# Optimization experiments

Measured on AMD Instinct MI355X. Metric: run time of the kernel, lower is better.

Reference implementation:

```python
import jax, jax.numpy as jnp
import numpy as np

# Module hyperparameters (from init_kwargs)
H, F = 8, 32            # num_heads, attention_filters
RY, RX = 3, 3           # spatial_radius
PH, PW = 2 * RY + 1, 2 * RX + 1
S = PH * PW             # patch_size = 49
HF = H * F


def setup_inputs() -> dict:
    key = jax.random.key(0)
    ks = jax.random.split(key, 6)
    B, Y, X, C = 4, 64, 64, 256
    x = jax.random.normal(ks[0], (B, Y, X, C), jnp.float32)
    # 1x1 conv kernels == dense matrices over the channel dim (no bias)
    Wq = jax.random.normal(ks[1], (C, HF), jnp.float32) / np.sqrt(C)
    Wk = jax.random.normal(ks[2], (C, HF), jnp.float32) / np.sqrt(C)
    Wv = jax.random.normal(ks[3], (C, HF), jnp.float32) / np.sqrt(C)
    Wo = jax.random.normal(ks[4], (HF, C), jnp.float32) / np.sqrt(HF)
    pos_emb = jax.random.normal(ks[5], (S, HF), jnp.float32) * 0.02
    return {"x": x, "Wq": Wq, "Wk": Wk, "Wv": Wv, "Wo": Wo, "pos_emb": pos_emb}


def reference(x, Wq, Wk, Wv, Wo, pos_emb):
    B, Y, X, C = x.shape
    dtype = x.dtype
    # 1x1 conv projections
    Q = x @ Wq                       # (B,Y,X,HF)
    K = x @ Wk
    V = x @ Wv
    # clipped patch centers (borders reuse interior patches)
    cy = jnp.clip(jnp.arange(Y), RY, Y - RY - 1)   # (Y,)
    cx = jnp.clip(jnp.arange(X), RX, X - RX - 1)   # (X,)
    # query relative-position indices within its patch
    qy = jnp.arange(Y) - cy + RY
    qx = jnp.arange(X) - cx + RX
    qidx = qy[:, None] * PW + qx[None, :]          # (Y,X) in [0,S)
    Q = Q + pos_emb[qidx]                          # add query pos embedding (HF)
    Q = Q.reshape(B, Y, X, H, F)
    K = K.reshape(B, Y, X, H, F)
    V = V.reshape(B, Y, X, H, F)
    cy_g, cx_g = jnp.meshgrid(cy, cx, indexing="ij")  # (Y,X)
    scale = jnp.asarray(1.0 / np.sqrt(F), dtype)
    NEG = jnp.asarray(-1e9, dtype)
    m = jnp.full((B, Y, X, H, 1), NEG, dtype)      # running max
    l = jnp.zeros((B, Y, X, H, 1), dtype)          # running sum-exp
    acc = jnp.zeros((B, Y, X, H, F), dtype)        # running value accumulator
    dy_vec = np.arange(-RY, RY + 1)                # within-chunk offsets ('col' mode)
    for dx in range(-RX, RX + 1):                  # chunk loop over columns (7 chunks)
        ny = jnp.clip(cy_g[None, :, :] + dy_vec[:, None, None], 0, Y - 1)  # (PH,Y,X)
        nx = jnp.clip(cx_g[None, :, :] + dx, 0, X - 1)                     # (1,Y,X)
        nx = jnp.broadcast_to(nx, ny.shape)
        sidx = (dy_vec + RY) * PW + (dx + RX)      # (PH,) relative-pos indices
        # gather neighbor K/V: (B,PH,Y,X,H,F)
        Kc = K[:, ny, nx] + pos_emb[sidx].reshape(PH, 1, 1, H, F)
        Vc = V[:, ny, nx]
        sc = jnp.einsum("byxhf,bsyxhf->byxhs", Q, Kc) * scale  # (B,Y,X,H,PH)
        new_m = jnp.maximum(m, sc.max(axis=-1, keepdims=True))
        alpha = jnp.exp(m - new_m)
        p = jnp.exp(sc - new_m)
        l = l * alpha + p.sum(axis=-1, keepdims=True)
        acc = acc * alpha + jnp.einsum("byxhs,bsyxhf->byxhf", p, Vc)
        m = new_m
    out = (acc / (l + 1e-8)).reshape(B, Y, X, HF) @ Wo
    return out
```

## Files before the change

kernel.cpp:

```cpp
#include <hip/hip_runtime.h>
#include <hip/hip_bf16.h>

static constexpr int NPOS = 4 * 64 * 64;
static constexpr int CD   = 256;
static constexpr int VSTR = 16416;
#define QSCALE (0.17677669529663687f * 1.4426950408889634f)

typedef __attribute__((ext_vector_type(8))) short bf16x8;
typedef __attribute__((ext_vector_type(4))) float f32x4;

__device__ __forceinline__ float bf2f(unsigned short u) {
    return __uint_as_float((unsigned int)u << 16);
}
__device__ __forceinline__ unsigned short bfbits(float f) {
    union { __hip_bfloat16 h; unsigned short u; } cv;
    cv.h = __float2bfloat16(f);
    return cv.u;
}
__device__ __forceinline__ unsigned int packbf2(float lo, float hi) {
    union { __hip_bfloat162 h; unsigned int u; } cv;
    cv.h.x = __float2bfloat16(lo);
    cv.h.y = __float2bfloat16(hi);
    return cv.u;
}
__device__ __forceinline__ uint4 pack8(float4 a, float4 b) {
    uint4 u;
    u.x = packbf2(a.x, a.y); u.y = packbf2(a.z, a.w);
    u.z = packbf2(b.x, b.y); u.w = packbf2(b.z, b.w);
    return u;
}
__device__ __forceinline__ void pl32swap(unsigned &a, unsigned &b) {
    auto r = __builtin_amdgcn_permlane32_swap(a, b, false, false);
    a = r[0]; b = r[1];
}
__device__ __forceinline__ void pl16swap(unsigned &a, unsigned &b) {
    auto r = __builtin_amdgcn_permlane16_swap(a, b, false, false);
    a = r[0]; b = r[1];
}

__global__ __launch_bounds__(256) void convert_kernel(
    const float* __restrict__ Wq, const float* __restrict__ Wk,
    const float* __restrict__ Wv, const float* __restrict__ Wo,
    const float* __restrict__ pe,
    __hip_bfloat16* __restrict__ Wfrag,
    __hip_bfloat16* __restrict__ pebf,
    __hip_bfloat16* __restrict__ Wofrag)
{
    int t = blockIdx.x * 256 + threadIdx.x;
    if (t < 24576) {
        int L = t & 63, ng = (t >> 6) & 7, s = (t >> 9) & 7, T = t >> 12;
        int mat = T >> 1;
        const float* src = (mat == 0) ? Wq : (mat == 1) ? Wk : Wv;
        int ncol  = (T & 1) * 128 + ng * 16 + (L & 15);
        int kbase = s * 32 + (L >> 4) * 8;
        __hip_bfloat16* dst = Wfrag + ((size_t)((T * 8 + s) * 8 + ng) * 64 + L) * 8;
#pragma unroll
        for (int j = 0; j < 8; ++j)
            dst[j] = __float2bfloat16(src[(kbase + j) * 256 + ncol]);
    } else if (t < 26624) {
        int u = t - 24576;
        int L = u & 63, Tn = (u >> 6) & 3, h = u >> 8;
        int s = Tn * 16 + (L & 15);
        int kbase = (L >> 4) * 8;
        __hip_bfloat16* dst = pebf + ((size_t)((h * 4 + Tn) * 64 + L)) * 8;
#pragma unroll
        for (int j = 0; j < 8; ++j) {
            float v = (s < 49) ? pe[s * 256 + h * 32 + kbase + j] * QSCALE : 0.f;
            dst[j] = __float2bfloat16(v);
        }
    } else if (t < 34816) {
        int u = t - 26624;
        int L = u & 63, ng = (u >> 6) & 7, s = (u >> 9) & 7, T = (u >> 12) & 1;
        int ncol  = T * 128 + ng * 16 + (L & 15);
        int kbase = s * 32 + (L >> 4) * 8;
        __hip_bfloat16* dst = Wofrag + ((size_t)((T * 8 + s) * 8 + ng) * 64 + L) * 8;
#pragma unroll
        for (int j = 0; j < 8; ++j)
            dst[j] = __float2bfloat16(Wo[(kbase + j) * 256 + ncol]);
    }
}

__global__ __launch_bounds__(768, 3) void qkv_mfma(
    const float* __restrict__ x,
    const __hip_bfloat16* __restrict__ Wfrag,
    const float* __restrict__ pe,
    unsigned short* __restrict__ QA,
    unsigned short* __restrict__ Kd,
    unsigned short* __restrict__ Vt)
{
    __shared__ __align__(16) unsigned short smem[256 * 68];
    unsigned short* As = smem;
    const int t = threadIdx.x;
    const int rowbase = blockIdx.x * 64;
    const int L = t & 63;
    const int w = t >> 6;
    const int quad = L >> 4, lrow = L & 15;
    const int T = w >> 1;
    const int ngb = (w & 1) * 4;
    const int g = T >> 1;
    const int lw = w & 3;

#pragma unroll
    for (int idx = t; idx < 2048; idx += 768) {
        const int row = idx >> 5, ch8 = idx & 31;
        const float* src = x + (size_t)(rowbase + row) * CD + ch8 * 8;
        float4 f0 = ((const float4*)src)[0];
        float4 f1 = ((const float4*)src)[1];
        *(uint4*)&As[row * 264 + ch8 * 8] = pack8(f0, f1);
    }

    f32x4 acc[4][4];
#pragma unroll
    for (int i = 0; i < 4; ++i)
#pragma unroll
        for (int j = 0; j < 4; ++j) acc[i][j] = (f32x4){0.f, 0.f, 0.f, 0.f};

    const __hip_bfloat16* wbase = Wfrag + ((size_t)(T * 64 + ngb) * 64 + L) * 8;
    bf16x8 bfr[4];
#pragma unroll
    for (int j = 0; j < 4; ++j)
        bfr[j] = *(const bf16x8*)(wbase + (size_t)j * 64 * 8);

    __syncthreads();

#pragma unroll
    for (int s = 0; s < 8; ++s) {
        bf16x8 nbfr[4];
        if (s < 7) {
#pragma unroll
            for (int j = 0; j < 4; ++j)
                nbfr[j] = *(const bf16x8*)(wbase + (size_t)((s + 1) * 8 + j) * 64 * 8);
        }
#pragma unroll
        for (int i = 0; i < 4; ++i) {
            bf16x8 af = *(const bf16x8*)&As[(i * 16 + lrow) * 264 + s * 32 + quad * 8];
#pragma unroll
            for (int j = 0; j < 4; ++j)
                acc[i][j] = __builtin_amdgcn_mfma_f32_16x16x32_bf16(af, bfr[j], acc[i][j], 0, 0, 0);
        }
#pragma unroll
        for (int j = 0; j < 4; ++j) bfr[j] = nbfr[j];
    }

    __syncthreads();

    if (g == 0) {
#pragma unroll
        for (int i = 0; i < 4; ++i)
#pragma unroll
            for (int r = 0; r < 4; ++r) {
                int row = rowbase + i * 16 + quad * 4 + r;
                int yy = (row >> 6) & 63, xx = row & 63;
                int cy = min(max(yy, 3), 60), cx = min(max(xx, 3), 60);
                int qidx = (yy - cy + 3) * 7 + (xx - cx + 3);
#pragma unroll
                for (int j = 0; j < 4; ++j) {
                    int c = lw * 64 + j * 16 + lrow;
                    QA[(size_t)row * CD + c] = bfbits(acc[i][j][r] + pe[qidx * 256 + c]);
                }
            }
    } else if (g == 1) {
#pragma unroll
        for (int i = 0; i < 4; ++i)
#pragma unroll
            for (int r = 0; r < 4; ++r) {
                int row = rowbase + i * 16 + quad * 4 + r;
#pragma unroll
                for (int j = 0; j < 4; ++j) {
                    int c = lw * 64 + j * 16 + lrow;
                    Kd[(size_t)row * CD + c] = bfbits(acc[i][j][r] * QSCALE);
                }
            }
    } else {
        unsigned short* vt = smem;
#pragma unroll
        for (int i = 0; i < 4; ++i)
#pragma unroll
            for (int j = 0; j < 4; ++j) {
                int c = lw * 64 + j * 16 + lrow;
                int row0 = i * 16 + quad * 4;
                *(unsigned int*)&vt[c * 68 + row0] =
                    (unsigned int)bfbits(acc[i][j][0]) | ((unsigned int)bfbits(acc[i][j][1]) << 16);
                *(unsigned int*)&vt[c * 68 + row0 + 2] =
                    (unsigned int)bfbits(acc[i][j][2]) | ((unsigned int)bfbits(acc[i][j][3]) << 16);
            }
    }
    __syncthreads();

    if (g == 2) {
        const int t4 = t - 512;
        const int grp = t4 >> 4, lig = t4 & 15;
        const int row_off = lig * 4;
        unsigned short* vt = smem;
#pragma unroll
        for (int pass = 0; pass < 16; ++pass) {
            int c = pass * 16 + grp;
            *(ushort4*)(Vt + (size_t)c * VSTR + rowbase + row_off) =
                *(const ushort4*)&vt[c * 68 + row_off];
        }
    }
}

__global__ __launch_bounds__(512) void attn_oproj(
    const unsigned short* __restrict__ QA,
    const unsigned short* __restrict__ Kd,
    const unsigned short* __restrict__ Vt,
    const __hip_bfloat16* __restrict__ pebf,
    const __hip_bfloat16* __restrict__ Wofrag,
    float* __restrict__ out)
{
    __shared__ __align__(16) unsigned short qpes[8][16 * 72];
    __shared__ __align__(16) unsigned short At[16 * 264];
    const int t = threadIdx.x, w = t >> 6, L = t & 63;
    const int lrow = L & 15, quad = L >> 4;
    const int bid = blockIdx.x;
    const int tile = ((bid & 7) << 7) | (bid >> 3);
    const int pos0 = tile * 16;
    const int x0 = pos0 & 63;
    const int yy = (pos0 >> 6) & 63, bb = pos0 >> 12;
    const int cy = min(max(yy, 3), 60);
    const int h = w;

    const int kc0 = min(max(x0 - 8 + lrow, 0), 63);
    const int kc1 = min(max(x0 + 8 + lrow, 0), 63);
    const f32x4 zero = {0.f, 0.f, 0.f, 0.f};
    unsigned short* qp = qpes[w];

    const int cx = min(max(x0 + lrow, 3), 60) - x0 + 5;
    int qiA[4], qiB[4];
    float mkA[4], mkB[4];
#pragma unroll
    for (int r = 0; r < 4; ++r) {
        const int sl = quad * 4 + r;
        int dxa = sl - cx;
        qiA[r] = lrow * 72 + min(max(dxa, 0), 6);
        mkA[r] = ((unsigned)dxa <= 6u) ? 1.f : 0.f;
        int dxb = 16 + sl - cx;
        qiB[r] = lrow * 72 + min(max(dxb, 0), 6);
        mkB[r] = ((unsigned)dxb <= 6u) ? 1.f : 0.f;
    }

    const bf16x8 qa = *(const bf16x8*)(QA + (size_t)(pos0 + lrow) * 256 + h * 32 + quad * 8);

#pragma unroll
    for (int Tn = 0; Tn < 4; ++Tn) {
        bf16x8 bp = *(const bf16x8*)(pebf + ((size_t)((h * 4 + Tn) * 64 + L)) * 8);
        f32x4 c = __builtin_amdgcn_mfma_f32_16x16x32_bf16(bp, qa, zero, 0, 0, 0);
        *(unsigned int*)&qp[lrow * 72 + Tn * 16 + quad * 4]     = packbf2(c[0], c[1]);
        *(unsigned int*)&qp[lrow * 72 + Tn * 16 + quad * 4 + 2] = packbf2(c[2], c[3]);
    }
    __builtin_amdgcn_s_waitcnt(0xc07f);

    float lacc = 0.f;
    f32x4 oT0 = zero, oT1 = zero;
    int rowpos = bb * 4096 + (cy - 3) * 64;

    const size_t koff = h * 32 + quad * 8;
    const size_t voff0 = (size_t)(h * 32 + lrow) * VSTR + x0 - 8 + quad * 8;
    const size_t voff1 = (size_t)(h * 32 + 16 + lrow) * VSTR + x0 - 8 + quad * 8;
    bf16x8 bk0 = *(const bf16x8*)(Kd + (size_t)(rowpos + kc0) * 256 + koff);
    bf16x8 bk1 = *(const bf16x8*)(Kd + (size_t)(rowpos + kc1) * 256 + koff);
    bf16x8 bv0 = *(const bf16x8*)(Vt + voff0 + rowpos);
    bf16x8 bv1 = *(const bf16x8*)(Vt + voff1 + rowpos);

    int qpofs = 0;
    for (int dy = 0; dy < 7; ++dy) {
        const int rnext = rowpos + 64;
        bf16x8 nk0, nk1, nv0, nv1;
        if (dy < 6) {
            nk0 = *(const bf16x8*)(Kd + (size_t)(rnext + kc0) * 256 + koff);
            nk1 = *(const bf16x8*)(Kd + (size_t)(rnext + kc1) * 256 + koff);
            nv0 = *(const bf16x8*)(Vt + voff0 + rnext);
            nv1 = *(const bf16x8*)(Vt + voff1 + rnext);
        }
        f32x4 s0 = __builtin_amdgcn_mfma_f32_16x16x32_bf16(bk0, qa, zero, 0, 0, 0);
        f32x4 s1 = __builtin_amdgcn_mfma_f32_16x16x32_bf16(bk1, qa, zero, 0, 0, 0);
        float e00 = exp2f(s0[0] + bf2f(qp[qiA[0] + qpofs])) * mkA[0];
        float e01 = exp2f(s0[1] + bf2f(qp[qiA[1] + qpofs])) * mkA[1];
        float e02 = exp2f(s0[2] + bf2f(qp[qiA[2] + qpofs])) * mkA[2];
        float e03 = exp2f(s0[3] + bf2f(qp[qiA[3] + qpofs])) * mkA[3];
        float e10 = exp2f(s1[0] + bf2f(qp[qiB[0] + qpofs])) * mkB[0];
        float e11 = exp2f(s1[1] + bf2f(qp[qiB[1] + qpofs])) * mkB[1];
        float e12 = exp2f(s1[2] + bf2f(qp[qiB[2] + qpofs])) * mkB[2];
        float e13 = exp2f(s1[3] + bf2f(qp[qiB[3] + qpofs])) * mkB[3];
        lacc += ((e00 + e01) + (e02 + e03)) + ((e10 + e11) + (e12 + e13));

        unsigned p0 = packbf2(e00, e01), p1 = packbf2(e02, e03);
        unsigned z0 = packbf2(e10, e11), z1 = packbf2(e12, e13);
        pl32swap(p0, z0);
        pl16swap(p0, z0);
        pl32swap(p1, z1);
        pl16swap(p1, z1);
        union { unsigned u[4]; bf16x8 v; } pb;
        pb.u[0] = p0; pb.u[1] = p1; pb.u[2] = z0; pb.u[3] = z1;

        oT0 = __builtin_amdgcn_mfma_f32_16x16x32_bf16(bv0, pb.v, oT0, 0, 0, 0);
        oT1 = __builtin_amdgcn_mfma_f32_16x16x32_bf16(bv1, pb.v, oT1, 0, 0, 0);
        bk0 = nk0; bk1 = nk1; bv0 = nv0; bv1 = nv1;
        rowpos = rnext;
        qpofs += 7;
    }

    lacc += __shfl_xor(lacc, 16);
    lacc += __shfl_xor(lacc, 32);
    const float inv = 1.f / (lacc + 1e-8f);

    {
        const int base = lrow * 264 + h * 32 + quad * 4;
        *(unsigned int*)&At[base]          = packbf2(oT0[0] * inv, oT0[1] * inv);
        *(unsigned int*)&At[base + 2]      = packbf2(oT0[2] * inv, oT0[3] * inv);
        *(unsigned int*)&At[base + 16]     = packbf2(oT1[0] * inv, oT1[1] * inv);
        *(unsigned int*)&At[base + 16 + 2] = packbf2(oT1[2] * inv, oT1[3] * inv);
    }
    __syncthreads();

    const int T = w >> 2;
    const int ngb = (w & 3) * 2;
    f32x4 acc[2];
    acc[0] = zero; acc[1] = zero;

#pragma unroll
    for (int s = 0; s < 8; ++s) {
        bf16x8 bfr[2];
#pragma unroll
        for (int j = 0; j < 2; ++j)
            bfr[j] = *(const bf16x8*)(Wofrag +
                      ((size_t)((T * 8 + s) * 8 + ngb + j) * 64 + L) * 8);
        bf16x8 af = *(const bf16x8*)(At + lrow * 264 + s * 32 + quad * 8);
#pragma unroll
        for (int j = 0; j < 2; ++j)
            acc[j] = __builtin_amdgcn_mfma_f32_16x16x32_bf16(af, bfr[j], acc[j], 0, 0, 0);
    }

#pragma unroll
    for (int r = 0; r < 4; ++r) {
        int row = pos0 + quad * 4 + r;
#pragma unroll
        for (int j = 0; j < 2; ++j) {
            int c = w * 32 + j * 16 + lrow;
            out[(size_t)row * CD + c] = acc[j][r];
        }
    }
}

extern "C" void kernel_launch(void* const* d_in, const int* in_sizes, int n_in,
                              void* d_out, int out_size, void* d_ws, size_t ws_size,
                              hipStream_t stream)
{
    const float* x  = (const float*)d_in[0];
    const float* Wq = (const float*)d_in[1];
    const float* Wk = (const float*)d_in[2];
    const float* Wv = (const float*)d_in[3];
    const float* Wo = (const float*)d_in[4];
    const float* pe = (const float*)d_in[5];
    float* out = (float*)d_out;

    char* ws = (char*)d_ws;
    unsigned short* QA = (unsigned short*)ws;
    unsigned short* Kd = (unsigned short*)(ws + (8u << 20));
    unsigned short* Vt = (unsigned short*)(ws + (16u << 20));
    char* fr = ws + (25u << 20) + 4096;
    __hip_bfloat16* Wfrag  = (__hip_bfloat16*)fr;
    __hip_bfloat16* pebf   = (__hip_bfloat16*)(fr + (384u << 10));
    __hip_bfloat16* Wofrag = (__hip_bfloat16*)(fr + (416u << 10));

    convert_kernel<<<136, 256, 0, stream>>>(Wq, Wk, Wv, Wo, pe, Wfrag, pebf, Wofrag);
    qkv_mfma<<<256, 768, 0, stream>>>(x, Wfrag, pe, QA, Kd, Vt);
    attn_oproj<<<1024, 512, 0, stream>>>(QA, Kd, Vt, pebf, Wofrag, out);
}
```

Baseline: 121.9 us.

## Process two adjacent query rows per attention block to share K/V loads

Each attn_oproj block now handles two vertically adjacent 16-position rows. The K/V rows they share are loaded once and fed to both tiles over 7 or 8 iterations, instead of 7 per tile. Each Wo fragment loaded in the output projection is also reused for both tiles, and the grid is halved to 512 blocks with a launch-bounds occupancy hint added. This cuts global K/V and Wo traffic, at the cost of more registers and shared memory per block and fewer blocks to fill the GPU.

New measurement: 114.6 us. 1.06x faster.

```diff
diff --git a/kernel.cpp b/kernel.cpp
--- a/kernel.cpp
+++ b/kernel.cpp
@@ -201,7 +201,7 @@
     }
 }
 
-__global__ __launch_bounds__(512) void attn_oproj(
+__global__ __launch_bounds__(512, 4) void attn_oproj(
     const unsigned short* __restrict__ QA,
     const unsigned short* __restrict__ Kd,
     const unsigned short* __restrict__ Vt,
@@ -209,22 +209,29 @@
     const __hip_bfloat16* __restrict__ Wofrag,
     float* __restrict__ out)
 {
-    __shared__ __align__(16) unsigned short qpes[8][16 * 72];
-    __shared__ __align__(16) unsigned short At[16 * 264];
+    __shared__ __align__(16) unsigned short qpes[8 * 2 * 1152];
+    __shared__ __align__(16) unsigned short At[2 * 16 * 264];
     const int t = threadIdx.x, w = t >> 6, L = t & 63;
     const int lrow = L & 15, quad = L >> 4;
     const int bid = blockIdx.x;
-    const int tile = ((bid & 7) << 7) | (bid >> 3);
-    const int pos0 = tile * 16;
-    const int x0 = pos0 & 63;
-    const int yy = (pos0 >> 6) & 63, bb = pos0 >> 12;
-    const int cy = min(max(yy, 3), 60);
+    const int p = ((bid & 7) << 6) | (bid >> 3);
+    const int b = p >> 7, ypair = (p >> 2) & 31, x0 = (p & 3) * 16;
+    const int yyA = ypair * 2;
+    const int pos0a = b * 4096 + yyA * 64 + x0;
+    const int pos0b = pos0a + 64;
+    const int cyA = min(max(yyA, 3), 60);
+    const int cyB = min(max(yyA + 1, 3), 60);
+    const int d = cyB - cyA;
+    const int nit = 7 + d;
     const int h = w;
 
     const int kc0 = min(max(x0 - 8 + lrow, 0), 63);
     const int kc1 = min(max(x0 + 8 + lrow, 0), 63);
     const f32x4 zero = {0.f, 0.f, 0.f, 0.f};
-    unsigned short* qp = qpes[w];
+    unsigned short* qpA = qpes + w * 2304;
+    unsigned short* qpB = qpA + 1152;
+    unsigned short* At_a = At;
+    unsigned short* At_b = At + 16 * 264;
 
     const int cx = min(max(x0 + lrow, 3), 60) - x0 + 5;
     int qiA[4], qiB[4];
@@ -240,20 +247,24 @@
         mkB[r] = ((unsigned)dxb <= 6u) ? 1.f : 0.f;
     }
 
-    const bf16x8 qa = *(const bf16x8*)(QA + (size_t)(pos0 + lrow) * 256 + h * 32 + quad * 8);
+    const bf16x8 qaA = *(const bf16x8*)(QA + (size_t)(pos0a + lrow) * 256 + h * 32 + quad * 8);
+    const bf16x8 qaB = *(const bf16x8*)(QA + (size_t)(pos0b + lrow) * 256 + h * 32 + quad * 8);
 
 #pragma unroll
     for (int Tn = 0; Tn < 4; ++Tn) {
         bf16x8 bp = *(const bf16x8*)(pebf + ((size_t)((h * 4 + Tn) * 64 + L)) * 8);
-        f32x4 c = __builtin_amdgcn_mfma_f32_16x16x32_bf16(bp, qa, zero, 0, 0, 0);
-        *(unsigned int*)&qp[lrow * 72 + Tn * 16 + quad * 4]     = packbf2(c[0], c[1]);
-        *(unsigned int*)&qp[lrow * 72 + Tn * 16 + quad * 4 + 2] = packbf2(c[2], c[3]);
+        f32x4 cA = __builtin_amdgcn_mfma_f32_16x16x32_bf16(bp, qaA, zero, 0, 0, 0);
+        f32x4 cB = __builtin_amdgcn_mfma_f32_16x16x32_bf16(bp, qaB, zero, 0, 0, 0);
+        *(unsigned int*)&qpA[lrow * 72 + Tn * 16 + quad * 4]     = packbf2(cA[0], cA[1]);
+        *(unsigned int*)&qpA[lrow * 72 + Tn * 16 + quad * 4 + 2] = packbf2(cA[2], cA[3]);
+        *(unsigned int*)&qpB[lrow * 72 + Tn * 16 + quad * 4]     = packbf2(cB[0], cB[1]);
+        *(unsigned int*)&qpB[lrow * 72 + Tn * 16 + quad * 4 + 2] = packbf2(cB[2], cB[3]);
     }
     __builtin_amdgcn_s_waitcnt(0xc07f);
 
-    float lacc = 0.f;
-    f32x4 oT0 = zero, oT1 = zero;
-    int rowpos = bb * 4096 + (cy - 3) * 64;
+    float laccA = 0.f, laccB = 0.f;
+    f32x4 o0a = zero, o1a = zero, o0b = zero, o1b = zero;
+    int rowpos = b * 4096 + (cyA - 3) * 64;
 
     const size_t koff = h * 32 + quad * 8;
     const size_t voff0 = (size_t)(h * 32 + lrow) * VSTR + x0 - 8 + quad * 8;
@@ -263,61 +274,69 @@
     bf16x8 bv0 = *(const bf16x8*)(Vt + voff0 + rowpos);
     bf16x8 bv1 = *(const bf16x8*)(Vt + voff1 + rowpos);
 
-    int qpofs = 0;
-    for (int dy = 0; dy < 7; ++dy) {
+    auto tilestep = [&](const bf16x8& qa_, const unsigned short* qp_, int qpofs,
+                        float& lacc_, f32x4& o0_, f32x4& o1_) {
+        f32x4 s0 = __builtin_amdgcn_mfma_f32_16x16x32_bf16(bk0, qa_, zero, 0, 0, 0);
+        f32x4 s1 = __builtin_amdgcn_mfma_f32_16x16x32_bf16(bk1, qa_, zero, 0, 0, 0);
+        float e00 = exp2f(s0[0] + bf2f(qp_[qiA[0] + qpofs])) * mkA[0];
+        float e01 = exp2f(s0[1] + bf2f(qp_[qiA[1] + qpofs])) * mkA[1];
+        float e02 = exp2f(s0[2] + bf2f(qp_[qiA[2] + qpofs])) * mkA[2];
+        float e03 = exp2f(s0[3] + bf2f(qp_[qiA[3] + qpofs])) * mkA[3];
+        float e10 = exp2f(s1[0] + bf2f(qp_[qiB[0] + qpofs])) * mkB[0];
+        float e11 = exp2f(s1[1] + bf2f(qp_[qiB[1] + qpofs])) * mkB[1];
+        float e12 = exp2f(s1[2] + bf2f(qp_[qiB[2] + qpofs])) * mkB[2];
+        float e13 = exp2f(s1[3] + bf2f(qp_[qiB[3] + qpofs])) * mkB[3];
+        lacc_ += ((e00 + e01) + (e02 + e03)) + ((e10 + e11) + (e12 + e13));
+        unsigned p0 = packbf2(e00, e01), p1 = packbf2(e02, e03);
+        unsigned z0 = packbf2(e10, e11), z1 = packbf2(e12, e13);
+        pl32swap(p0, z0); pl16swap(p0, z0);
+        pl32swap(p1, z1); pl16swap(p1, z1);
+        union { unsigned u[4]; bf16x8 v; } pb;
+        pb.u[0] = p0; pb.u[1] = p1; pb.u[2] = z0; pb.u[3] = z1;
+        o0_ = __builtin_amdgcn_mfma_f32_16x16x32_bf16(bv0, pb.v, o0_, 0, 0, 0);
+        o1_ = __builtin_amdgcn_mfma_f32_16x16x32_bf16(bv1, pb.v, o1_, 0, 0, 0);
+    };
+
+    for (int i = 0; i < nit; ++i) {
         const int rnext = rowpos + 64;
         bf16x8 nk0, nk1, nv0, nv1;
-        if (dy < 6) {
+        if (i < nit - 1) {
             nk0 = *(const bf16x8*)(Kd + (size_t)(rnext + kc0) * 256 + koff);
             nk1 = *(const bf16x8*)(Kd + (size_t)(rnext + kc1) * 256 + koff);
             nv0 = *(const bf16x8*)(Vt + voff0 + rnext);
             nv1 = *(const bf16x8*)(Vt + voff1 + rnext);
         }
-        f32x4 s0 = __builtin_amdgcn_mfma_f32_16x16x32_bf16(bk0, qa, zero, 0, 0, 0);
-        f32x4 s1 = __builtin_amdgcn_mfma_f32_16x16x32_bf16(bk1, qa, zero, 0, 0, 0);
-        float e00 = exp2f(s0[0] + bf2f(qp[qiA[0] + qpofs])) * mkA[0];
-        float e01 = exp2f(s0[1] + bf2f(qp[qiA[1] + qpofs])) * mkA[1];
-        float e02 = exp2f(s0[2] + bf2f(qp[qiA[2] + qpofs])) * mkA[2];
-        float e03 = exp2f(s0[3] + bf2f(qp[qiA[3] + qpofs])) * mkA[3];
-        float e10 = exp2f(s1[0] + bf2f(qp[qiB[0] + qpofs])) * mkB[0];
-        float e11 = exp2f(s1[1] + bf2f(qp[qiB[1] + qpofs])) * mkB[1];
-        float e12 = exp2f(s1[2] + bf2f(qp[qiB[2] + qpofs])) * mkB[2];
-        float e13 = exp2f(s1[3] + bf2f(qp[qiB[3] + qpofs])) * mkB[3];
-        lacc += ((e00 + e01) + (e02 + e03)) + ((e10 + e11) + (e12 + e13));
-
-        unsigned p0 = packbf2(e00, e01), p1 = packbf2(e02, e03);
-        unsigned z0 = packbf2(e10, e11), z1 = packbf2(e12, e13);
-        pl32swap(p0, z0);
-        pl16swap(p0, z0);
-        pl32swap(p1, z1);
-        pl16swap(p1, z1);
-        union { unsigned u[4]; bf16x8 v; } pb;
-        pb.u[0] = p0; pb.u[1] = p1; pb.u[2] = z0; pb.u[3] = z1;
-
-        oT0 = __builtin_amdgcn_mfma_f32_16x16x32_bf16(bv0, pb.v, oT0, 0, 0, 0);
-        oT1 = __builtin_amdgcn_mfma_f32_16x16x32_bf16(bv1, pb.v, oT1, 0, 0, 0);
+        if (i < 7)
+            tilestep(qaA, qpA, i * 7, laccA, o0a, o1a);
+        if (i >= d)
+            tilestep(qaB, qpB, (i - d) * 7, laccB, o0b, o1b);
         bk0 = nk0; bk1 = nk1; bv0 = nv0; bv1 = nv1;
         rowpos = rnext;
-        qpofs += 7;
-    }
-
-    lacc += __shfl_xor(lacc, 16);
-    lacc += __shfl_xor(lacc, 32);
-    const float inv = 1.f / (lacc + 1e-8f);
-
+    }
+
+    laccA += __shfl_xor(laccA, 16);
+    laccA += __shfl_xor(laccA, 32);
+    laccB += __shfl_xor(laccB, 16);
+    laccB += __shfl_xor(laccB, 32);
+    const float invA = 1.f / (laccA + 1e-8f);
+    const float invB = 1.f / (laccB + 1e-8f);
     {
         const int base = lrow * 264 + h * 32 + quad * 4;
-        *(unsigned int*)&At[base]          = packbf2(oT0[0] * inv, oT0[1] * inv);
-        *(unsigned int*)&At[base + 2]      = packbf2(oT0[2] * inv, oT0[3] * inv);
-        *(unsigned int*)&At[base + 16]     = packbf2(oT1[0] * inv, oT1[1] * inv);
-        *(unsigned int*)&At[base + 16 + 2] = packbf2(oT1[2] * inv, oT1[3] * inv);
+        *(unsigned int*)&At_a[base]          = packbf2(o0a[0] * invA, o0a[1] * invA);
+        *(unsigned int*)&At_a[base + 2]      = packbf2(o0a[2] * invA, o0a[3] * invA);
+        *(unsigned int*)&At_a[base + 16]     = packbf2(o1a[0] * invA, o1a[1] * invA);
+        *(unsigned int*)&At_a[base + 16 + 2] = packbf2(o1a[2] * invA, o1a[3] * invA);
+        *(unsigned int*)&At_b[base]          = packbf2(o0b[0] * invB, o0b[1] * invB);
+        *(unsigned int*)&At_b[base + 2]      = packbf2(o0b[2] * invB, o0b[3] * invB);
+        *(unsigned int*)&At_b[base + 16]     = packbf2(o1b[0] * invB, o1b[1] * invB);
+        *(unsigned int*)&At_b[base + 16 + 2] = packbf2(o1b[2] * invB, o1b[3] * invB);
     }
     __syncthreads();
 
     const int T = w >> 2;
     const int ngb = (w & 3) * 2;
-    f32x4 acc[2];
-    acc[0] = zero; acc[1] = zero;
+    f32x4 accA[2], accB[2];
+    accA[0] = zero; accA[1] = zero; accB[0] = zero; accB[1] = zero;
 
 #pragma unroll
     for (int s = 0; s < 8; ++s) {
@@ -326,19 +345,24 @@
         for (int j = 0; j < 2; ++j)
             bfr[j] = *(const bf16x8*)(Wofrag +
                       ((size_t)((T * 8 + s) * 8 + ngb + j) * 64 + L) * 8);
-        bf16x8 af = *(const bf16x8*)(At + lrow * 264 + s * 32 + quad * 8);
-#pragma unroll
-        for (int j = 0; j < 2; ++j)
-            acc[j] = __builtin_amdgcn_mfma_f32_16x16x32_bf16(af, bfr[j], acc[j], 0, 0, 0);
+        bf16x8 afA = *(const bf16x8*)(At_a + lrow * 264 + s * 32 + quad * 8);
+        bf16x8 afB = *(const bf16x8*)(At_b + lrow * 264 + s * 32 + quad * 8);
+#pragma unroll
+        for (int j = 0; j < 2; ++j) {
+            accA[j] = __builtin_amdgcn_mfma_f32_16x16x32_bf16(afA, bfr[j], accA[j], 0, 0, 0);
+            accB[j] = __builtin_amdgcn_mfma_f32_16x16x32_bf16(afB, bfr[j], accB[j], 0, 0, 0);
+        }
     }
 
 #pragma unroll
     for (int r = 0; r < 4; ++r) {
-        int row = pos0 + quad * 4 + r;
+        int rowA = pos0a + quad * 4 + r;
+        int rowB = pos0b + quad * 4 + r;
 #pragma unroll
         for (int j = 0; j < 2; ++j) {
             int c = w * 32 + j * 16 + lrow;
-            out[(size_t)row * CD + c] = acc[j][r];
+            out[(size_t)rowA * CD + c] = accA[j][r];
+            out[(size_t)rowB * CD + c] = accB[j][r];
         }
     }
 }
@@ -366,5 +390,5 @@
 
     convert_kernel<<<136, 256, 0, stream>>>(Wq, Wk, Wv, Wo, pe, Wfrag, pebf, Wofrag);
     qkv_mfma<<<256, 768, 0, stream>>>(x, Wfrag, pe, QA, Kd, Vt);
-    attn_oproj<<<1024, 512, 0, stream>>>(QA, Kd, Vt, pebf, Wofrag, out);
-}
+    attn_oproj<<<512, 512, 0, stream>>>(QA, Kd, Vt, pebf, Wofrag, out);
+}
```
